# Performance work log

Measured on AMD Instinct MI355X. Metric: run time of the kernel, lower is better.

## Reference

```python
import jax, jax.numpy as jnp
import numpy as np

N = 20000   # nodes
E = 160000  # edges
G = 64      # graphs in batch
DIN = 128
DIMS = [(128, 256), (256, 256), (256, 512), (512, 512), (512, 256), (256, 256)]


def setup_inputs() -> dict:
    key = jax.random.key(0)
    ks = jax.random.split(key, 3 + 3 * len(DIMS) + 2)
    inp = {}
    inp["x"] = jax.random.normal(ks[0], (N, DIN), jnp.float32)
    inp["edge_index"] = jax.random.randint(ks[1], (2, E), 0, N)
    inp["batch"] = jnp.sort(jax.random.randint(ks[2], (N,), 0, G))
    i = 3
    for li, (din, dout) in enumerate(DIMS, 1):
        s = 1.0 / np.sqrt(din)
        inp[f"Wl{li}"] = jax.random.normal(ks[i], (din, dout), jnp.float32) * s; i += 1
        inp[f"bl{li}"] = jnp.zeros((dout,), jnp.float32); i += 1
        inp[f"Wr{li}"] = jax.random.normal(ks[i], (din, dout), jnp.float32) * s; i += 1
    inp["Wlin"] = jax.random.normal(ks[i], (256, 6), jnp.float32) * (1.0 / 16.0); i += 1
    inp["blin"] = jnp.zeros((6,), jnp.float32)
    return inp


def _sage_conv(x, src, dst, Wl, bl, Wr):
    # PyG SAGEConv: out = lin_l(mean_{j in N(i)} x_j) + lin_r(x_i); bias lives in lin_l.
    msgs = x[src]                                              # [E, din] gather
    agg = jax.ops.segment_sum(msgs, dst, num_segments=N)       # [N, din]
    deg = jax.ops.segment_sum(jnp.ones((src.shape[0],), x.dtype), dst, num_segments=N)
    agg = agg / jnp.clip(deg, 1.0)[:, None]                    # mean aggregation
    return agg @ Wl + bl + x @ Wr


def _segment_mean(x, seg, num_segments):
    s = jax.ops.segment_sum(x, seg, num_segments=num_segments)
    cnt = jax.ops.segment_sum(jnp.ones((x.shape[0],), x.dtype), seg, num_segments=num_segments)
    return s / jnp.clip(cnt, 1.0)[:, None]


def reference(x, edge_index, batch,
              Wl1, bl1, Wr1, Wl2, bl2, Wr2, Wl3, bl3, Wr3,
              Wl4, bl4, Wr4, Wl5, bl5, Wr5, Wl6, bl6, Wr6,
              Wlin, blin):
    src, dst = edge_index[0], edge_index[1]
    slope = 0.01  # F.leaky_relu default negative slope
    h = x
    params = [(Wl1, bl1, Wr1), (Wl2, bl2, Wr2), (Wl3, bl3, Wr3),
              (Wl4, bl4, Wr4), (Wl5, bl5, Wr5), (Wl6, bl6, Wr6)]
    for li, (Wl, bl, Wr) in enumerate(params):
        h = _sage_conv(h, src, dst, Wl, bl, Wr)
        if li < 5:  # no activation after conv6
            h = jnp.where(h >= 0, h, slope * h)
    g = _segment_mean(h, batch, G)  # global_mean_pool -> [G, 256]
    # F.dropout(training=False) is identity in eval mode
    return g @ Wlin + blin
```

## Files before the change

kernel.cpp:

```cpp
#include <hip/hip_runtime.h>

#define NN 20000
#define MP 20096
#define NE 160000
#define NG 64

typedef __attribute__((ext_vector_type(8))) short bf16x8;
typedef __attribute__((ext_vector_type(4))) float f32x4;

__device__ __forceinline__ short f2bf_hi(float x) {
    unsigned u = __float_as_uint(x);
    return (short)((u + 0x7FFFu + ((u >> 16) & 1u)) >> 16);
}

__device__ __forceinline__ float bf2f(short h) {
    return __uint_as_float(((unsigned)(unsigned short)h) << 16);
}

typedef const __attribute__((address_space(1))) unsigned int* as1_u32p;
typedef __attribute__((address_space(3))) unsigned int* as3_u32p;
__device__ __forceinline__ void gll16(const void* g, void* l) {
    __builtin_amdgcn_global_load_lds((as1_u32p)g, (as3_u32p)l, 16, 0, 0);
}

struct WDesc { const float* W; short* Wh; int K; int dout; int tstart; };
struct WPack { WDesc d[10]; };

#define HIST_BLOCKS 625
#define XBF_BLOCKS 1250
#define WCONV_BASE (HIST_BLOCKS + XBF_BLOCKS)

__global__ __launch_bounds__(256) void prep_kernel(WPack p,
                                                   const int* __restrict__ dst,
                                                   int* __restrict__ deg,
                                                   const float* __restrict__ x,
                                                   short* __restrict__ xh) {
    __shared__ float tile[32][33];
    int bid = blockIdx.x;
    int t = threadIdx.x;
    if (bid < HIST_BLOCKS) {
        int e = bid * 256 + t;
        atomicAdd(&deg[dst[e]], 1);
        return;
    }
    if (bid < WCONV_BASE) {
        int i = (bid - HIST_BLOCKS) * 256 + t;
        float4 a = *(const float4*)&x[(size_t)i * 8];
        float4 b = *(const float4*)&x[(size_t)i * 8 + 4];
        bf16x8 v;
        v[0] = f2bf_hi(a.x); v[1] = f2bf_hi(a.y); v[2] = f2bf_hi(a.z); v[3] = f2bf_hi(a.w);
        v[4] = f2bf_hi(b.x); v[5] = f2bf_hi(b.y); v[6] = f2bf_hi(b.z); v[7] = f2bf_hi(b.w);
        *(bf16x8*)&xh[(size_t)i * 8] = v;
        return;
    }
    int wb = bid - WCONV_BASE;
    int i = 0;
    #pragma unroll
    for (int k = 1; k < 10; ++k)
        if (wb >= p.d[k].tstart) i = k;
    const float* W = p.d[i].W;
    short* Wh = p.d[i].Wh;
    int K = p.d[i].K, dout = p.d[i].dout;
    int local = wb - p.d[i].tstart;
    int ntk = K >> 5;
    int kb = (local % ntk) * 32, nb = (local / ntk) * 32;
    int lr = t >> 5, lc = t & 31;
    #pragma unroll
    for (int r = 0; r < 4; ++r)
        tile[lr + r * 8][lc] = W[(size_t)(kb + lr + r * 8) * dout + nb + lc];
    __syncthreads();
    int nn = t >> 3, kq = (t & 7) * 4;
    short4 h;
    h.x = f2bf_hi(tile[kq + 0][nn]);
    h.y = f2bf_hi(tile[kq + 1][nn]);
    h.z = f2bf_hi(tile[kq + 2][nn]);
    h.w = f2bf_hi(tile[kq + 3][nn]);
    *(short4*)&Wh[(size_t)(nb + nn) * K + kb + kq] = h;
}

#define SCAN_BLOCKS 20

__global__ void scan_part(const int* __restrict__ deg, int* __restrict__ bsum) {
    __shared__ int wsum[16];
    int b = blockIdx.x, t = threadIdx.x;
    int i = b * 1024 + t;
    int v = (i < NN) ? deg[i] : 0;
    int lane = t & 63, w = t >> 6;
    int s = v;
    #pragma unroll
    for (int off = 1; off < 64; off <<= 1) s += __shfl_xor(s, off, 64);
    if (lane == 0) wsum[w] = s;
    __syncthreads();
    if (t == 0) {
        int tot = 0;
        #pragma unroll
        for (int k = 0; k < 16; ++k) tot += wsum[k];
        bsum[b] = tot;
    }
}

__global__ void scan_mid(const int* __restrict__ bsum, int* __restrict__ boff,
                         int* __restrict__ rowptr) {
    int t = threadIdx.x;
    int v = (t < SCAN_BLOCKS) ? bsum[t] : 0;
    int s = v;
    #pragma unroll
    for (int off = 1; off < 64; off <<= 1) {
        int u = __shfl_up(s, off, 64);
        if (t >= off) s += u;
    }
    if (t < SCAN_BLOCKS) boff[t] = s - v;
    if (t == SCAN_BLOCKS - 1) rowptr[NN] = s;
}

__global__ void scan_fin(const int* __restrict__ deg, const int* __restrict__ boff,
                         int* __restrict__ rowptr) {
    __shared__ int wsum[16];
    int b = blockIdx.x, t = threadIdx.x;
    int i = b * 1024 + t;
    int v = (i < NN) ? deg[i] : 0;
    int lane = t & 63, w = t >> 6;
    int s = v;
    #pragma unroll
    for (int off = 1; off < 64; off <<= 1) {
        int u = __shfl_up(s, off, 64);
        if (lane >= off) s += u;
    }
    if (lane == 63) wsum[w] = s;
    __syncthreads();
    if (w == 0 && lane < 16) {
        int ws = wsum[lane];
        #pragma unroll
        for (int off = 1; off < 16; off <<= 1) {
            int u = __shfl_up(ws, off, 64);
            if (lane >= off) ws += u;
        }
        wsum[lane] = ws;
    }
    __syncthreads();
    int wpre = (w > 0) ? wsum[w - 1] : 0;
    if (i < NN) rowptr[i] = boff[b] + wpre + s - v;
}

__global__ void fill_kernel(const int* __restrict__ src, const int* __restrict__ dst,
                            const int* __restrict__ rowptr, const int* __restrict__ deg,
                            int* __restrict__ wcount, int* __restrict__ col,
                            float* __restrict__ wgt) {
    int e = blockIdx.x * 256 + threadIdx.x;
    if (e < NE) {
        int d = dst[e];
        int p = rowptr[d] + atomicAdd(&wcount[d], 1);
        col[p] = src[e];
        wgt[p] = 1.f / fmaxf((float)deg[d], 1.f);
    }
}

__global__ __launch_bounds__(256, 4) void gemm_mfma(
    const short* __restrict__ A,
    const short* __restrict__ Bh,
    short* __restrict__ P1, short* __restrict__ P2,
    int M, int K, int dout, int ncsh) {
    __shared__ short lds[2][2][4096];
    int tid = threadIdx.x;
    int lane = tid & 63, w = tid >> 6;
    int wm = w >> 1, wn = w & 1;

    int nwg = gridDim.x;
    int q = nwg >> 3, r = nwg & 7;
    int xcd = blockIdx.x & 7, idx = blockIdx.x >> 3;
    int swz = (xcd < r ? xcd * (q + 1) : r * (q + 1) + (xcd - r) * q) + idx;
    int mblk = (swz >> ncsh) << 7;
    int nblk = (swz & ((1 << ncsh) - 1)) << 7;

    int rl = lane >> 2;
    int gchunk = (lane & 3) ^ ((lane >> 3) & 3);
    int nsteps = K >> 5;

    auto stage = [&](int b, int t) {
        int kc = t << 5;
        short* L = &lds[b][0][0];
        size_t ko = (size_t)kc + gchunk * 8;
        #pragma unroll
        for (int qq = 0; qq < 2; ++qq) {
            int row = w * 32 + qq * 16;
            int gr = row + rl;
            gll16(A  + (size_t)(mblk + gr) * K + ko, L + 0 * 4096 + row * 32);
            gll16(Bh + (size_t)(nblk + gr) * K + ko, L + 1 * 4096 + row * 32);
        }
    };

    f32x4 acc[4][4] = {};
    int chunk_sw = (((lane >> 4) ^ ((lane >> 1) & 3))) << 3;
    int ar = (wm << 6) + (lane & 15);
    int br = (wn << 6) + (lane & 15);

    stage(0, 0);
    stage(1, 1);
    for (int t = 0; t < nsteps; ++t) {
        int b = t & 1;
        if (t < nsteps - 1) asm volatile("s_waitcnt vmcnt(4)" ::: "memory");
        else                asm volatile("s_waitcnt vmcnt(0)" ::: "memory");
        __builtin_amdgcn_s_barrier();
        __builtin_amdgcn_sched_barrier(0);
        const short* L = &lds[b][0][0];
        bf16x8 av[4], bv[4];
        #pragma unroll
        for (int i = 0; i < 4; ++i) {
            av[i] = *(const bf16x8*)(L + 0 * 4096 + (ar + i * 16) * 32 + chunk_sw);
            bv[i] = *(const bf16x8*)(L + 1 * 4096 + (br + i * 16) * 32 + chunk_sw);
        }
        #pragma unroll
        for (int i = 0; i < 4; ++i)
            #pragma unroll
            for (int j = 0; j < 4; ++j)
                acc[i][j] = __builtin_amdgcn_mfma_f32_16x16x32_bf16(av[i], bv[j], acc[i][j], 0, 0, 0);
        __builtin_amdgcn_sched_barrier(0);
        __builtin_amdgcn_s_barrier();
        __builtin_amdgcn_sched_barrier(0);
        if (t + 2 < nsteps) stage(b, t + 2);
    }

    int crow = mblk + (wm << 6) + ((lane >> 4) << 2);
    int ccol = nblk + (wn << 6) + (lane & 15);
    bool is_p1 = (nblk < dout);
    short* P = is_p1 ? P1 : P2;
    int cbase = is_p1 ? ccol : (ccol - dout);
    #pragma unroll
    for (int i = 0; i < 4; ++i) {
        #pragma unroll
        for (int r = 0; r < 4; ++r) {
            int gm = crow + i * 16 + r;
            if (gm >= M) continue;
            #pragma unroll
            for (int j = 0; j < 4; ++j)
                P[(size_t)gm * dout + cbase + j * 16] = f2bf_hi(acc[i][j][r]);
        }
    }
}

template <int DOUT>
__global__ __launch_bounds__(256) void agg_post(
    const short* __restrict__ P1, const short* __restrict__ P2,
    const float* __restrict__ bias,
    const int* __restrict__ rowptr, const int* __restrict__ col,
    short* __restrict__ oh) {
    constexpr int TPN = DOUT / 8;
    constexpr int NPB = 256 / TPN;
    int node = blockIdx.x * NPB + threadIdx.x / TPN;
    if (node >= NN) return;
    int t = threadIdx.x % TPN;
    int s = rowptr[node], e = rowptr[node + 1];
    float acc[8] = {};
    for (int j0 = s; j0 < e; j0 += 8) {
        int idx[8];
        #pragma unroll
        for (int k = 0; k < 8; ++k) {
            int jj = j0 + k;
            idx[k] = col[(jj < e) ? jj : s];
        }
        bf16x8 v[8];
        #pragma unroll
        for (int k = 0; k < 8; ++k)
            v[k] = *(const bf16x8*)&P1[(size_t)idx[k] * DOUT + t * 8];
        #pragma unroll
        for (int k = 0; k < 8; ++k) {
            float msk = (j0 + k < e) ? 1.f : 0.f;
            #pragma unroll
            for (int m = 0; m < 8; ++m)
                acc[m] += msk * bf2f(v[k][m]);
        }
    }
    float inv = 1.f / fmaxf((float)(e - s), 1.f);
    bf16x8 p2 = *(const bf16x8*)&P2[(size_t)node * DOUT + t * 8];
    float4 ba = *(const float4*)&bias[t * 8];
    float4 bb = *(const float4*)&bias[t * 8 + 4];
    float bv[8] = {ba.x, ba.y, ba.z, ba.w, bb.x, bb.y, bb.z, bb.w};
    bf16x8 vh;
    #pragma unroll
    for (int m = 0; m < 8; ++m) {
        float c = acc[m] * inv + bf2f(p2[m]) + bv[m];
        c = (c >= 0.f) ? c : 0.01f * c;
        vh[m] = f2bf_hi(c);
    }
    *(bf16x8*)&oh[(size_t)node * DOUT + t * 8] = vh;
}

#define ESPLIT 32
__global__ __launch_bounds__(256) void sgather(const short* __restrict__ h5,
                                               const int* __restrict__ batch,
                                               const int* __restrict__ rowptr,
                                               const int* __restrict__ col,
                                               const float* __restrict__ wgt,
                                               float* __restrict__ ap) {
    int gi = blockIdx.x, c = blockIdx.y;
    int t = threadIdx.x;
    int lo = 0, hi = NN;
    while (lo < hi) { int m = (lo + hi) >> 1; if (batch[m] < gi) lo = m + 1; else hi = m; }
    int start = lo;
    hi = NN;
    while (lo < hi) { int m = (lo + hi) >> 1; if (batch[m] < gi + 1) lo = m + 1; else hi = m; }
    int end = lo;
    int e0 = rowptr[start], e1 = rowptr[end];
    int L = e1 - e0;
    int ps = e0 + (int)(((long)L * c) / ESPLIT);
    int pe = e0 + (int)(((long)L * (c + 1)) / ESPLIT);
    float acc = 0.f;
    int p = ps;
    for (; p + 4 <= pe; p += 4) {
        int c0 = col[p], c1 = col[p + 1], c2 = col[p + 2], c3 = col[p + 3];
        float w0 = wgt[p], w1 = wgt[p + 1], w2 = wgt[p + 2], w3 = wgt[p + 3];
        float a0 = bf2f(h5[(size_t)c0 * 256 + t]);
        float a1 = bf2f(h5[(size_t)c1 * 256 + t]);
        float a2 = bf2f(h5[(size_t)c2 * 256 + t]);
        float a3 = bf2f(h5[(size_t)c3 * 256 + t]);
        acc += (w0 * a0 + w1 * a1) + (w2 * a2 + w3 * a3);
    }
    for (; p < pe; ++p)
        acc += wgt[p] * bf2f(h5[(size_t)col[p] * 256 + t]);
    if (pe > ps) atomicAdd(&ap[gi * 256 + t], acc);
}

#define PSPLIT 16
__global__ __launch_bounds__(256) void pool_h(const short* __restrict__ h5,
                                              const int* __restrict__ batch,
                                              float* __restrict__ hp, int* __restrict__ gcnt) {
    int gi = blockIdx.x, c = blockIdx.y;
    int t = threadIdx.x;
    int lo = 0, hi = NN;
    while (lo < hi) { int m = (lo + hi) >> 1; if (batch[m] < gi) lo = m + 1; else hi = m; }
    int start = lo;
    hi = NN;
    while (lo < hi) { int m = (lo + hi) >> 1; if (batch[m] < gi + 1) lo = m + 1; else hi = m; }
    int end = lo;
    int L = end - start;
    if (c == 0 && t == 0) gcnt[gi] = L;
    int cs = start + (int)(((long)L * c) / PSPLIT);
    int ce = start + (int)(((long)L * (c + 1)) / PSPLIT);
    float acc = 0.f;
    for (int n = cs; n < ce; ++n) acc += bf2f(h5[(size_t)n * 256 + t]);
    if (ce > cs) atomicAdd(&hp[gi * 256 + t], acc);
}

__global__ __launch_bounds__(256) void head_kernel(
    const float* __restrict__ ap, const float* __restrict__ hp,
    const int* __restrict__ gcnt,
    const float* __restrict__ Wl6, const float* __restrict__ Wr6,
    const float* __restrict__ bl6,
    const float* __restrict__ Wlin, const float* __restrict__ blin,
    float* __restrict__ out) {
    __shared__ float a_s[256], h_s[256], t6[256];
    int g = blockIdx.x, t = threadIdx.x;
    float inv = 1.f / fmaxf((float)gcnt[g], 1.f);
    a_s[t] = ap[g * 256 + t] * inv;
    h_s[t] = hp[g * 256 + t] * inv;
    __syncthreads();
    float acc = 0.f;
    for (int k = 0; k < 256; ++k)
        acc += a_s[k] * Wl6[k * 256 + t] + h_s[k] * Wr6[k * 256 + t];
    t6[t] = acc + bl6[t];
    __syncthreads();
    if (t < 6) {
        float s = 0.f;
        for (int k = 0; k < 256; ++k) s += t6[k] * Wlin[k * 6 + t];
        out[g * 6 + t] = s + blin[t];
    }
}

extern "C" void kernel_launch(void* const* d_in, const int* in_sizes, int n_in,
                              void* d_out, int out_size, void* d_ws, size_t ws_size,
                              hipStream_t stream) {
    const float* x = (const float*)d_in[0];
    const int* ei = (const int*)d_in[1];
    const int* batch = (const int*)d_in[2];
    const float *Wl[6], *bl[6], *Wr[6];
    for (int l = 0; l < 6; ++l) {
        Wl[l] = (const float*)d_in[3 + 3 * l];
        bl[l] = (const float*)d_in[4 + 3 * l];
        Wr[l] = (const float*)d_in[5 + 3 * l];
    }
    const float* Wlin = (const float*)d_in[21];
    const float* blin = (const float*)d_in[22];
    float* out = (float*)d_out;

    char* ws = (char*)d_ws;
    size_t off = 0;
    auto alloc = [&](size_t bytes) {
        void* p = ws + off;
        off += (bytes + 255) & ~(size_t)255;
        return p;
    };
    short* xh   = (short*)alloc((size_t)MP * 128 * 2);
    short* hA   = (short*)alloc((size_t)MP * 512 * 2);
    short* hB   = (short*)alloc((size_t)MP * 512 * 2);
    short* P1   = (short*)alloc((size_t)MP * 512 * 2);
    short* P2   = (short*)alloc((size_t)MP * 512 * 2);
    int* col    = (int*)alloc((size_t)NE * 4);
    float* wgt  = (float*)alloc((size_t)NE * 4);
    int* bsum   = (int*)alloc(64 * 4);
    int* boff   = (int*)alloc(64 * 4);
    float* ap   = (float*)alloc((size_t)NG * 256 * 4);
    float* hp   = (float*)alloc((size_t)NG * 256 * 4);
    int* deg    = (int*)alloc((size_t)NN * 4);
    int* wcount = (int*)alloc((size_t)NN * 4);
    int* gcnt   = (int*)alloc((size_t)NG * 4);
    int* rowptr = (int*)alloc((size_t)(NN + 1) * 4);
    short* wtbuf = (short*)alloc((size_t)4 * 688128 * 2);
    (void)ws_size; (void)in_sizes; (void)n_in; (void)out_size;

    size_t zero_bytes = (size_t)((char*)gcnt - (char*)ap) + NG * 4;
    hipMemsetAsync((void*)ap, 0, zero_bytes, stream);

    const int* src = ei;
    const int* dst = ei + NE;

    const int dins[5]  = {128, 256, 256, 512, 512};
    const int douts[5] = {256, 256, 512, 512, 256};

    short* Bth[5];
    int tcum = 0;
    {
        WPack pack;
        short* p = wtbuf;
        for (int l = 0; l < 5; ++l) {
            size_t half = (size_t)dins[l] * douts[l];
            int ntiles = (dins[l] / 32) * (douts[l] / 32);
            Bth[l] = p; p += 2 * half;
            pack.d[2 * l]     = { Wl[l], Bth[l],        dins[l], douts[l], tcum }; tcum += ntiles;
            pack.d[2 * l + 1] = { Wr[l], Bth[l] + half, dins[l], douts[l], tcum }; tcum += ntiles;
        }
        prep_kernel<<<WCONV_BASE + tcum, 256, 0, stream>>>(pack, dst, deg, x, xh);
    }

    scan_part<<<SCAN_BLOCKS, 1024, 0, stream>>>(deg, bsum);
    scan_mid<<<1, 64, 0, stream>>>(bsum, boff, rowptr);
    scan_fin<<<SCAN_BLOCKS, 1024, 0, stream>>>(deg, boff, rowptr);
    fill_kernel<<<(NE + 255) / 256, 256, 0, stream>>>(src, dst, rowptr, deg, wcount, col, wgt);

    const short* cur = xh;
    short* hbuf[2] = {hA, hB};
    for (int l = 0; l < 5; ++l) {
        int K = dins[l], dout = douts[l];
        int ncol = (2 * dout) >> 7;
        int ncsh = (ncol == 4) ? 2 : 3;
        int nwg = (MP / 128) * ncol;
        gemm_mfma<<<nwg, 256, 0, stream>>>(cur, Bth[l], P1, P2, NN, K, dout, ncsh);
        if (dout == 256)
            agg_post<256><<<(NN + 7) / 8, 256, 0, stream>>>(P1, P2, bl[l], rowptr, col, hbuf[l & 1]);
        else
            agg_post<512><<<(NN + 3) / 4, 256, 0, stream>>>(P1, P2, bl[l], rowptr, col, hbuf[l & 1]);
        cur = hbuf[l & 1];
    }

    dim3 egrid(NG, ESPLIT);
    sgather<<<egrid, 256, 0, stream>>>(cur, batch, rowptr, col, wgt, ap);
    dim3 pgrid(NG, PSPLIT);
    pool_h<<<pgrid, 256, 0, stream>>>(cur, batch, hp, gcnt);
    head_kernel<<<NG, 256, 0, stream>>>(ap, hp, gcnt, Wl[5], Wr[5], bl[5], Wlin, blin, out);
}
```

Before: 380.6 us.

## Aggregate before transform in layers 1-4 with concatenated-K GEMM epilogue

For layers 1-4, the mean aggregation of neighbor features now happens first in a separate gather kernel. A single GEMM then runs over the concatenated [agg | h] inputs against stacked [Wl; Wr] weights, with bias and leaky-ReLU fused into its epilogue. Before, each layer ran a GEMM producing two dout-wide products and a post-aggregation pass over them. This reorders gather and transform per layer: gathers now read din-wide rows rather than dout-wide rows, and the GEMM writes one output instead of two. The separate sgather and pool_h kernels are also merged into one tail kernel, and layer 5 keeps the old transform-then-aggregate path.

```diff
diff --git a/kernel.cpp b/kernel.cpp
--- a/kernel.cpp
+++ b/kernel.cpp
@@ -23,7 +23,7 @@
     __builtin_amdgcn_global_load_lds((as1_u32p)g, (as3_u32p)l, 16, 0, 0);
 }
 
-struct WDesc { const float* W; short* Wh; int K; int dout; int tstart; };
+struct WDesc { const float* W; short* Wh; int Kst; int koff; int K; int dout; int tstart; };
 struct WPack { WDesc d[10]; };
 
 #define HIST_BLOCKS 625
@@ -60,6 +60,7 @@
         if (wb >= p.d[k].tstart) i = k;
     const float* W = p.d[i].W;
     short* Wh = p.d[i].Wh;
+    int Kst = p.d[i].Kst, koff = p.d[i].koff;
     int K = p.d[i].K, dout = p.d[i].dout;
     int local = wb - p.d[i].tstart;
     int ntk = K >> 5;
@@ -75,7 +76,7 @@
     h.y = f2bf_hi(tile[kq + 1][nn]);
     h.z = f2bf_hi(tile[kq + 2][nn]);
     h.w = f2bf_hi(tile[kq + 3][nn]);
-    *(short4*)&Wh[(size_t)(nb + nn) * K + kb + kq] = h;
+    *(short4*)&Wh[(size_t)(nb + nn) * Kst + koff + kb + kq] = h;
 }
 
 #define SCAN_BLOCKS 20
@@ -155,11 +156,47 @@
     }
 }
 
-__global__ __launch_bounds__(256, 4) void gemm_mfma(
-    const short* __restrict__ A,
-    const short* __restrict__ Bh,
-    short* __restrict__ P1, short* __restrict__ P2,
-    int M, int K, int dout, int ncsh) {
+template <int K>
+__global__ __launch_bounds__(256) void agg_mean(
+    const short* __restrict__ h, const int* __restrict__ rowptr,
+    const int* __restrict__ col, short* __restrict__ agg) {
+    constexpr int TPN = K / 8;
+    constexpr int NPB = 256 / TPN;
+    int node = blockIdx.x * NPB + threadIdx.x / TPN;
+    if (node >= NN) return;
+    int t = threadIdx.x % TPN;
+    int s = rowptr[node], e = rowptr[node + 1];
+    float acc[8] = {};
+    for (int j0 = s; j0 < e; j0 += 8) {
+        int idx[8];
+        #pragma unroll
+        for (int k = 0; k < 8; ++k) {
+            int jj = j0 + k;
+            idx[k] = col[(jj < e) ? jj : s];
+        }
+        bf16x8 v[8];
+        #pragma unroll
+        for (int k = 0; k < 8; ++k)
+            v[k] = *(const bf16x8*)&h[(size_t)idx[k] * K + t * 8];
+        #pragma unroll
+        for (int k = 0; k < 8; ++k) {
+            float msk = (j0 + k < e) ? 1.f : 0.f;
+            #pragma unroll
+            for (int m = 0; m < 8; ++m)
+                acc[m] += msk * bf2f(v[k][m]);
+        }
+    }
+    float inv = 1.f / fmaxf((float)(e - s), 1.f);
+    bf16x8 vh;
+    #pragma unroll
+    for (int m = 0; m < 8; ++m) vh[m] = f2bf_hi(acc[m] * inv);
+    *(bf16x8*)&agg[(size_t)node * K + t * 8] = vh;
+}
+
+__global__ __launch_bounds__(256, 4) void gemm_af(
+    const short* __restrict__ A1, const short* __restrict__ A2,
+    const short* __restrict__ Bt, const float* __restrict__ bias,
+    short* __restrict__ H, int M, int K, int dout, int ncsh) {
     __shared__ short lds[2][2][4096];
     int tid = threadIdx.x;
     int lane = tid & 63, w = tid >> 6;
@@ -174,18 +211,23 @@
 
     int rl = lane >> 2;
     int gchunk = (lane & 3) ^ ((lane >> 3) & 3);
-    int nsteps = K >> 5;
+    int KK = K << 1;
+    int s1 = K >> 5;
+    int nsteps = KK >> 5;
 
     auto stage = [&](int b, int t) {
-        int kc = t << 5;
+        const short* A; int kc;
+        if (t < s1) { A = A1; kc = t << 5; }
+        else        { A = A2; kc = (t - s1) << 5; }
         short* L = &lds[b][0][0];
-        size_t ko = (size_t)kc + gchunk * 8;
+        size_t koA = (size_t)kc + gchunk * 8;
+        size_t koB = (size_t)(t << 5) + gchunk * 8;
         #pragma unroll
         for (int qq = 0; qq < 2; ++qq) {
             int row = w * 32 + qq * 16;
             int gr = row + rl;
-            gll16(A  + (size_t)(mblk + gr) * K + ko, L + 0 * 4096 + row * 32);
-            gll16(Bh + (size_t)(nblk + gr) * K + ko, L + 1 * 4096 + row * 32);
+            gll16(A  + (size_t)(mblk + gr) * K  + koA, L + 0 * 4096 + row * 32);
+            gll16(Bt + (size_t)(nblk + gr) * KK + koB, L + 1 * 4096 + row * 32);
         }
     };
 
@@ -193,6 +235,10 @@
     int chunk_sw = (((lane >> 4) ^ ((lane >> 1) & 3))) << 3;
     int ar = (wm << 6) + (lane & 15);
     int br = (wn << 6) + (lane & 15);
+    int ccol = nblk + (wn << 6) + (lane & 15);
+
+    float bv0 = bias[ccol], bv1 = bias[ccol + 16], bv2 = bias[ccol + 32], bv3 = bias[ccol + 48];
+    asm volatile("" : "+v"(bv0), "+v"(bv1), "+v"(bv2), "+v"(bv3));
 
     stage(0, 0);
     stage(1, 1);
@@ -221,6 +267,89 @@
     }
 
     int crow = mblk + (wm << 6) + ((lane >> 4) << 2);
+    float bvv[4] = {bv0, bv1, bv2, bv3};
+    #pragma unroll
+    for (int i = 0; i < 4; ++i) {
+        #pragma unroll
+        for (int r = 0; r < 4; ++r) {
+            int gm = crow + i * 16 + r;
+            if (gm >= M) continue;
+            #pragma unroll
+            for (int j = 0; j < 4; ++j) {
+                float c = acc[i][j][r] + bvv[j];
+                c = (c >= 0.f) ? c : 0.01f * c;
+                H[(size_t)gm * dout + ccol + j * 16] = f2bf_hi(c);
+            }
+        }
+    }
+}
+
+__global__ __launch_bounds__(256, 4) void gemm_gf(
+    const short* __restrict__ A,
+    const short* __restrict__ Bh,
+    short* __restrict__ P1, short* __restrict__ P2,
+    int M, int K, int dout, int ncsh) {
+    __shared__ short lds[2][2][4096];
+    int tid = threadIdx.x;
+    int lane = tid & 63, w = tid >> 6;
+    int wm = w >> 1, wn = w & 1;
+
+    int nwg = gridDim.x;
+    int q = nwg >> 3, r = nwg & 7;
+    int xcd = blockIdx.x & 7, idx = blockIdx.x >> 3;
+    int swz = (xcd < r ? xcd * (q + 1) : r * (q + 1) + (xcd - r) * q) + idx;
+    int mblk = (swz >> ncsh) << 7;
+    int nblk = (swz & ((1 << ncsh) - 1)) << 7;
+
+    int rl = lane >> 2;
+    int gchunk = (lane & 3) ^ ((lane >> 3) & 3);
+    int nsteps = K >> 5;
+
+    auto stage = [&](int b, int t) {
+        int kc = t << 5;
+        short* L = &lds[b][0][0];
+        size_t ko = (size_t)kc + gchunk * 8;
+        #pragma unroll
+        for (int qq = 0; qq < 2; ++qq) {
+            int row = w * 32 + qq * 16;
+            int gr = row + rl;
+            gll16(A  + (size_t)(mblk + gr) * K + ko, L + 0 * 4096 + row * 32);
+            gll16(Bh + (size_t)(nblk + gr) * K + ko, L + 1 * 4096 + row * 32);
+        }
+    };
+
+    f32x4 acc[4][4] = {};
+    int chunk_sw = (((lane >> 4) ^ ((lane >> 1) & 3))) << 3;
+    int ar = (wm << 6) + (lane & 15);
+    int br = (wn << 6) + (lane & 15);
+
+    stage(0, 0);
+    stage(1, 1);
+    for (int t = 0; t < nsteps; ++t) {
+        int b = t & 1;
+        if (t < nsteps - 1) asm volatile("s_waitcnt vmcnt(4)" ::: "memory");
+        else                asm volatile("s_waitcnt vmcnt(0)" ::: "memory");
+        __builtin_amdgcn_s_barrier();
+        __builtin_amdgcn_sched_barrier(0);
+        const short* L = &lds[b][0][0];
+        bf16x8 av[4], bv[4];
+        #pragma unroll
+        for (int i = 0; i < 4; ++i) {
+            av[i] = *(const bf16x8*)(L + 0 * 4096 + (ar + i * 16) * 32 + chunk_sw);
+            bv[i] = *(const bf16x8*)(L + 1 * 4096 + (br + i * 16) * 32 + chunk_sw);
+        }
+        #pragma unroll
+        for (int i = 0; i < 4; ++i)
+            #pragma unroll
+            for (int j = 0; j < 4; ++j)
+                acc[i][j] = __builtin_amdgcn_mfma_f32_16x16x32_bf16(av[i], bv[j], acc[i][j], 0, 0, 0);
+        __builtin_amdgcn_sched_barrier(0);
+        __builtin_amdgcn_s_barrier();
+        __builtin_amdgcn_sched_barrier(0);
+        if (t + 2 < nsteps) stage(b, t + 2);
+    }
+
+    int crow = mblk + (wm << 6) + ((lane >> 4) << 2);
     int ccol = nblk + (wn << 6) + (lane & 15);
     bool is_p1 = (nblk < dout);
     short* P = is_p1 ? P1 : P2;
@@ -238,15 +367,14 @@
     }
 }
 
-template <int DOUT>
-__global__ __launch_bounds__(256) void agg_post(
+__global__ __launch_bounds__(256) void agg_post256(
     const short* __restrict__ P1, const short* __restrict__ P2,
     const float* __restrict__ bias,
     const int* __restrict__ rowptr, const int* __restrict__ col,
     short* __restrict__ oh) {
+    constexpr int DOUT = 256;
     constexpr int TPN = DOUT / 8;
-    constexpr int NPB = 256 / TPN;
-    int node = blockIdx.x * NPB + threadIdx.x / TPN;
+    int node = blockIdx.x * 8 + threadIdx.x / TPN;
     if (node >= NN) return;
     int t = threadIdx.x % TPN;
     int s = rowptr[node], e = rowptr[node + 1];
@@ -286,12 +414,14 @@
 }
 
 #define ESPLIT 32
-__global__ __launch_bounds__(256) void sgather(const short* __restrict__ h5,
-                                               const int* __restrict__ batch,
-                                               const int* __restrict__ rowptr,
-                                               const int* __restrict__ col,
-                                               const float* __restrict__ wgt,
-                                               float* __restrict__ ap) {
+__global__ __launch_bounds__(256) void tail_pool(const short* __restrict__ h5,
+                                                 const int* __restrict__ batch,
+                                                 const int* __restrict__ rowptr,
+                                                 const int* __restrict__ col,
+                                                 const float* __restrict__ wgt,
+                                                 float* __restrict__ ap,
+                                                 float* __restrict__ hp,
+                                                 int* __restrict__ gcnt) {
     int gi = blockIdx.x, c = blockIdx.y;
     int t = threadIdx.x;
     int lo = 0, hi = NN;
@@ -300,6 +430,7 @@
     hi = NN;
     while (lo < hi) { int m = (lo + hi) >> 1; if (batch[m] < gi + 1) lo = m + 1; else hi = m; }
     int end = lo;
+    if (c == 0 && t == 0) gcnt[gi] = end - start;
     int e0 = rowptr[start], e1 = rowptr[end];
     int L = e1 - e0;
     int ps = e0 + (int)(((long)L * c) / ESPLIT);
@@ -318,27 +449,12 @@
     for (; p < pe; ++p)
         acc += wgt[p] * bf2f(h5[(size_t)col[p] * 256 + t]);
     if (pe > ps) atomicAdd(&ap[gi * 256 + t], acc);
-}
-
-#define PSPLIT 16
-__global__ __launch_bounds__(256) void pool_h(const short* __restrict__ h5,
-                                              const int* __restrict__ batch,
-                                              float* __restrict__ hp, int* __restrict__ gcnt) {
-    int gi = blockIdx.x, c = blockIdx.y;
-    int t = threadIdx.x;
-    int lo = 0, hi = NN;
-    while (lo < hi) { int m = (lo + hi) >> 1; if (batch[m] < gi) lo = m + 1; else hi = m; }
-    int start = lo;
-    hi = NN;
-    while (lo < hi) { int m = (lo + hi) >> 1; if (batch[m] < gi + 1) lo = m + 1; else hi = m; }
-    int end = lo;
-    int L = end - start;
-    if (c == 0 && t == 0) gcnt[gi] = L;
-    int cs = start + (int)(((long)L * c) / PSPLIT);
-    int ce = start + (int)(((long)L * (c + 1)) / PSPLIT);
-    float acc = 0.f;
-    for (int n = cs; n < ce; ++n) acc += bf2f(h5[(size_t)n * 256 + t]);
-    if (ce > cs) atomicAdd(&hp[gi * 256 + t], acc);
+    int Ln = end - start;
+    int cs = start + (int)(((long)Ln * c) / ESPLIT);
+    int ce = start + (int)(((long)Ln * (c + 1)) / ESPLIT);
+    float acch = 0.f;
+    for (int n = cs; n < ce; ++n) acch += bf2f(h5[(size_t)n * 256 + t]);
+    if (ce > cs) atomicAdd(&hp[gi * 256 + t], acch);
 }
 
 __global__ __launch_bounds__(256) void head_kernel(
@@ -392,8 +508,9 @@
     short* xh   = (short*)alloc((size_t)MP * 128 * 2);
     short* hA   = (short*)alloc((size_t)MP * 512 * 2);
     short* hB   = (short*)alloc((size_t)MP * 512 * 2);
-    short* P1   = (short*)alloc((size_t)MP * 512 * 2);
-    short* P2   = (short*)alloc((size_t)MP * 512 * 2);
+    short* aggb = (short*)alloc((size_t)MP * 512 * 2);
+    short* P1   = (short*)alloc((size_t)MP * 256 * 2);
+    short* P2   = (short*)alloc((size_t)MP * 256 * 2);
     int* col    = (int*)alloc((size_t)NE * 4);
     float* wgt  = (float*)alloc((size_t)NE * 4);
     int* bsum   = (int*)alloc(64 * 4);
@@ -416,17 +533,23 @@
     const int dins[5]  = {128, 256, 256, 512, 512};
     const int douts[5] = {256, 256, 512, 512, 256};
 
-    short* Bth[5];
+    short* Bt[5];
     int tcum = 0;
     {
         WPack pack;
         short* p = wtbuf;
         for (int l = 0; l < 5; ++l) {
-            size_t half = (size_t)dins[l] * douts[l];
-            int ntiles = (dins[l] / 32) * (douts[l] / 32);
-            Bth[l] = p; p += 2 * half;
-            pack.d[2 * l]     = { Wl[l], Bth[l],        dins[l], douts[l], tcum }; tcum += ntiles;
-            pack.d[2 * l + 1] = { Wr[l], Bth[l] + half, dins[l], douts[l], tcum }; tcum += ntiles;
+            int K = dins[l], dout = douts[l];
+            int ntiles = (K / 32) * (dout / 32);
+            if (l < 4) {
+                Bt[l] = p; p += (size_t)dout * 2 * K;
+                pack.d[2 * l]     = { Wl[l], Bt[l], 2 * K, 0, K, dout, tcum }; tcum += ntiles;
+                pack.d[2 * l + 1] = { Wr[l], Bt[l], 2 * K, K, K, dout, tcum }; tcum += ntiles;
+            } else {
+                Bt[l] = p; p += (size_t)2 * dout * K;
+                pack.d[2 * l]     = { Wl[l], Bt[l],                     K, 0, K, dout, tcum }; tcum += ntiles;
+                pack.d[2 * l + 1] = { Wr[l], Bt[l] + (size_t)dout * K,  K, 0, K, dout, tcum }; tcum += ntiles;
+            }
         }
         prep_kernel<<<WCONV_BASE + tcum, 256, 0, stream>>>(pack, dst, deg, x, xh);
     }
@@ -436,24 +559,18 @@
     scan_fin<<<SCAN_BLOCKS, 1024, 0, stream>>>(deg, boff, rowptr);
     fill_kernel<<<(NE + 255) / 256, 256, 0, stream>>>(src, dst, rowptr, deg, wcount, col, wgt);
 
-    const short* cur = xh;
-    short* hbuf[2] = {hA, hB};
-    for (int l = 0; l < 5; ++l) {
-        int K = dins[l], dout = douts[l];
-        int ncol = (2 * dout) >> 7;
-        int ncsh = (ncol == 4) ? 2 : 3;
-        int nwg = (MP / 128) * ncol;
-        gemm_mfma<<<nwg, 256, 0, stream>>>(cur, Bth[l], P1, P2, NN, K, dout, ncsh);
-        if (dout == 256)
-            agg_post<256><<<(NN + 7) / 8, 256, 0, stream>>>(P1, P2, bl[l], rowptr, col, hbuf[l & 1]);
-        else
-            agg_post<512><<<(NN + 3) / 4, 256, 0, stream>>>(P1, P2, bl[l], rowptr, col, hbuf[l & 1]);
-        cur = hbuf[l & 1];
-    }
-
-    dim3 egrid(NG, ESPLIT);
-    sgather<<<egrid, 256, 0, stream>>>(cur, batch, rowptr, col, wgt, ap);
-    dim3 pgrid(NG, PSPLIT);
-    pool_h<<<pgrid, 256, 0, stream>>>(cur, batch, hp, gcnt);
+    agg_mean<128><<<(NN + 15) / 16, 256, 0, stream>>>(xh, rowptr, col, aggb);
+    gemm_af<<<(MP / 128) * 2, 256, 0, stream>>>(aggb, xh, Bt[0], bl[0], hA, NN, 128, 256, 1);
+    agg_mean<256><<<(NN + 7) / 8, 256, 0, stream>>>(hA, rowptr, col, aggb);
+    gemm_af<<<(MP / 128) * 2, 256, 0, stream>>>(aggb, hA, Bt[1], bl[1], hB, NN, 256, 256, 1);
+    agg_mean<256><<<(NN + 7) / 8, 256, 0, stream>>>(hB, rowptr, col, aggb);
+    gemm_af<<<(MP / 128) * 4, 256, 0, stream>>>(aggb, hB, Bt[2], bl[2], hA, NN, 256, 512, 2);
+    agg_mean<512><<<(NN + 3) / 4, 256, 0, stream>>>(hA, rowptr, col, aggb);
+    gemm_af<<<(MP / 128) * 4, 256, 0, stream>>>(aggb, hA, Bt[3], bl[3], hB, NN, 512, 512, 2);
+    gemm_gf<<<(MP / 128) * 4, 256, 0, stream>>>(hB, Bt[4], P1, P2, NN, 512, 256, 2);
+    agg_post256<<<(NN + 7) / 8, 256, 0, stream>>>(P1, P2, bl[4], rowptr, col, hA);
+
+    dim3 tgrid(NG, ESPLIT);
+    tail_pool<<<tgrid, 256, 0, stream>>>(hA, batch, rowptr, col, wgt, ap, hp, gcnt);
     head_kernel<<<NG, 256, 0, stream>>>(ap, hp, gcnt, Wl[5], Wr[5], bl[5], Wlin, blin, out);
 }
```

New measurement: 346.3 us. -9.0%, faster.
